# Optimization experiments

Hardware: AMD Instinct MI355X
Metric: run time of the kernel (lower is better)

## Reference

```python
import jax, jax.numpy as jnp
import numpy as np

B, T, D, H, L, C = 64, 512, 256, 1024, 2, 128


def setup_inputs() -> dict:
    key = jax.random.key(0)
    ks = jax.random.split(key, 11)
    s = 0.05
    return {
        "x": jax.random.normal(ks[0], (B, T, D), dtype=jnp.float32),
        "W_ih0": jax.random.normal(ks[1], (4 * H, D), dtype=jnp.float32) * s,
        "W_hh0": jax.random.normal(ks[2], (4 * H, H), dtype=jnp.float32) * s,
        "b_ih0": jax.random.normal(ks[3], (4 * H,), dtype=jnp.float32) * s,
        "b_hh0": jax.random.normal(ks[4], (4 * H,), dtype=jnp.float32) * s,
        "W_ih1": jax.random.normal(ks[5], (4 * H, H), dtype=jnp.float32) * s,
        "W_hh1": jax.random.normal(ks[6], (4 * H, H), dtype=jnp.float32) * s,
        "b_ih1": jax.random.normal(ks[7], (4 * H,), dtype=jnp.float32) * s,
        "b_hh1": jax.random.normal(ks[8], (4 * H,), dtype=jnp.float32) * s,
        "W_fc": jax.random.normal(ks[9], (C, H), dtype=jnp.float32) * s,
        "b_fc": jax.random.normal(ks[10], (C,), dtype=jnp.float32) * s,
    }


def _lstm_cell(inp, h, c, Wi, Wh, bi, bh):
    # PyTorch LSTMCell: gates ordered i, f, g, o
    gates = inp @ Wi.T + bi + h @ Wh.T + bh  # [B, 4H]
    i, f, g, o = jnp.split(gates, 4, axis=-1)
    c_new = jax.nn.sigmoid(f) * c + jax.nn.sigmoid(i) * jnp.tanh(g)
    h_new = jax.nn.sigmoid(o) * jnp.tanh(c_new)
    return h_new, c_new


def reference(x, W_ih0, W_hh0, b_ih0, b_hh0, W_ih1, W_hh1, b_ih1, b_hh1, W_fc, b_fc):
    b = x.shape[0]
    h0 = jnp.zeros((b, H), x.dtype)
    init = (h0, h0, h0, h0)  # (h_l0, c_l0, h_l1, c_l1)

    def step(carry, x_t):
        h0_, c0_, h1_, c1_ = carry
        h0n, c0n = _lstm_cell(x_t, h0_, c0_, W_ih0, W_hh0, b_ih0, b_hh0)
        h1n, c1n = _lstm_cell(h0n, h1_, c1_, W_ih1, W_hh1, b_ih1, b_hh1)
        return (h0n, c0n, h1n, c1n), None

    xt = jnp.swapaxes(x, 0, 1)  # [T, B, D]
    (h0f, c0f, h1f, c1f), _ = jax.lax.scan(step, init, xt)
    return h1f @ W_fc.T + b_fc  # [B, num_classes]
```

## Files before the change

### kernel.cpp

```cpp
#include <hip/hip_runtime.h>
#include <hip/hip_bf16.h>

#define B_ 64
#define T_ 512
#define D_ 256
#define H_ 1024
#define RING 64
#define PS 260

typedef __attribute__((ext_vector_type(8))) short short8;
typedef __attribute__((ext_vector_type(4))) float floatx4;

__device__ __forceinline__ unsigned short f2bf(float f){
  unsigned u = __builtin_bit_cast(unsigned, f);
  u = (u + 0x7fffu + ((u >> 16) & 1u)) >> 16;
  return (unsigned short)u;
}

__device__ __forceinline__ short8 pack8(floatx4 a, floatx4 b){
  short8 r;
  r[0]=(short)f2bf(a[0]); r[1]=(short)f2bf(a[1]); r[2]=(short)f2bf(a[2]); r[3]=(short)f2bf(a[3]);
  r[4]=(short)f2bf(b[0]); r[5]=(short)f2bf(b[1]); r[6]=(short)f2bf(b[2]); r[7]=(short)f2bf(b[3]);
  return r;
}

__device__ __forceinline__ float sigm(float v){ return 1.f/(1.f+__expf(-v)); }
__device__ __forceinline__ float tanh_f(float v){ return 1.f - 2.f/(1.f+__expf(2.f*v)); }

__device__ __forceinline__ void gpoll(const unsigned long long* watch, unsigned tgt0, unsigned tgt1){
  if (!(tgt0 | tgt1)) return;
  long g = 0;
  for (;;){
    unsigned long long v = __hip_atomic_load(watch, __ATOMIC_RELAXED, __HIP_MEMORY_SCOPE_AGENT);
    unsigned v0 = (unsigned)v, v1 = (unsigned)(v >> 32);
    if (__all(v0 >= tgt0 && v1 >= tgt1)) break;
    if (++g > (1L<<24)) break;
  }
}

__device__ __forceinline__ void lspin(unsigned* flag, unsigned tgt){
  long g = 0;
  while (__hip_atomic_load(flag, __ATOMIC_RELAXED, __HIP_MEMORY_SCOPE_WORKGROUP) < tgt){
    if (++g > (1L<<24)) break;
  }
}


template<int LAYER>
__device__ __forceinline__ void run_lstm(
    const float* __restrict__ x,
    const float* __restrict__ Wi, const float* __restrict__ Wh,
    const float* __restrict__ bi, const float* __restrict__ bh,
    unsigned* seq, unsigned short* h0h, unsigned short* h1h, float* h1f,
    int jbase, int j, int half,
    float* partial , float* c_st , float* biasv ,
    unsigned* rdy)
{
  constexpr int KTOT = LAYER ? 2048 : 1280;
  constexpr int KW   = KTOT/8;
  constexpr int NK   = KW/32;
  constexpr int KA   = LAYER ? 1024 : 256;

  const int tid  = threadIdx.x;
  const int wave = tid >> 6;
  const int lane = tid & 63;
  const int ksl  = wave;
  const int n15  = lane & 15;
  const int kq   = (lane >> 4) * 8;

  short8 bfr[4][NK];
  #pragma unroll
  for (int nt = 0; nt < 4; nt++){
    int n   = nt*16 + n15;
    int row = (n >> 4)*H_ + jbase + (n & 15);
    #pragma unroll
    for (int ks = 0; ks < NK; ks++){
      int k = ksl*KW + ks*32 + kq;
      const float* s = (k < KA) ? (Wi + (size_t)row*KA + k)
                                : (Wh + (size_t)row*H_ + (k - KA));
      bfr[nt][ks] = pack8(*(const floatx4*)s, *(const floatx4*)(s + 4));
    }
  }
  if (tid < 64){
    int col = (tid >> 4)*H_ + jbase + (tid & 15);
    biasv[tid] = bi[col] + bh[col];
  }
  c_st[tid & 511] = 0.f;
  if (tid == 0){ rdy[0] = 0u; }
  __syncthreads();

  const unsigned long long* watch =
      (const unsigned long long*)seq + (size_t)(LAYER*2 + half)*512 + lane;
  unsigned* post0 = seq + (size_t)(0*2 + half)*1024 + (size_t)j*2 + LAYER;
  unsigned* post1 = seq + (size_t)(1*2 + half)*1024 + (size_t)j*2 + LAYER;

  for (int t = 0; t < T_; t++){
    floatx4 xraw[LAYER ? 1 : NK][2][2];
    if constexpr (LAYER == 0){
      #pragma unroll
      for (int ks = 0; ks < NK; ks++){
        const int kb = ksl*KW + ks*32;
        if (kb < D_){
          const int kk = kb + kq;
          #pragma unroll
          for (int mt = 0; mt < 2; mt++){
            const float* xs = x + ((size_t)(half*32 + mt*16 + n15)*T_ + t)*D_ + kk;
            xraw[ks][mt][0] = *(const floatx4*)xs;
            xraw[ks][mt][1] = *(const floatx4*)(xs + 4);
          }
        }
      }
    }

    if (wave == 0){
      unsigned tgt0, tgt1;
      if (LAYER == 0){
        tgt0 = (unsigned)t;
        tgt1 = (t >= RING) ? (unsigned)(t - RING + 1) : 0u;
      } else {
        tgt0 = (unsigned)(t + 1);
        tgt1 = (unsigned)t;
      }
      gpoll(watch, tgt0, tgt1);
      if (lane == 0) __hip_atomic_store(&rdy[0], (unsigned)(t + 1),
                                        __ATOMIC_RELAXED, __HIP_MEMORY_SCOPE_WORKGROUP);
    } else {
      lspin(&rdy[0], (unsigned)(t + 1));
    }
    __builtin_amdgcn_sched_barrier(0);

    floatx4 acc[2][4];
    #pragma unroll
    for (int mt = 0; mt < 2; mt++)
      #pragma unroll
      for (int nt = 0; nt < 4; nt++)
        acc[mt][nt] = (floatx4)0.f;

    const unsigned short* h0t = h0h + ((size_t)((LAYER ? t : (t-1)) & (RING-1)) << 16);
    const unsigned short* h1t = h1h + ((size_t)((t-1) & (RING-1)) << 16);

    #pragma unroll
    for (int ks = 0; ks < NK; ks++){
      const int kb = ksl*KW + ks*32;
      if (kb >= KA && t == 0) continue;
      const int kk = kb + kq;
      short8 afr[2];
      if constexpr (LAYER == 0){
        if (kb < D_){
          #pragma unroll
          for (int mt = 0; mt < 2; mt++)
            afr[mt] = pack8(xraw[ks][mt][0], xraw[ks][mt][1]);
        } else {
          const int hk = kk - D_;
          const unsigned short* p = h0t + ((hk >> 4) << 10) + (hk & 15);
          #pragma unroll
          for (int mt = 0; mt < 2; mt++)
            afr[mt] = *(const short8*)(p + ((half*32 + mt*16 + n15) << 4));
        }
      } else {
        const int hk = (kb < 1024) ? kk : (kk - 1024);
        const unsigned short* sb = (kb < 1024) ? h0t : h1t;
        const unsigned short* p = sb + ((hk >> 4) << 10) + (hk & 15);
        #pragma unroll
        for (int mt = 0; mt < 2; mt++)
          afr[mt] = *(const short8*)(p + ((half*32 + mt*16 + n15) << 4));
      }
      #pragma unroll
      for (int mt = 0; mt < 2; mt++)
        #pragma unroll
        for (int nt = 0; nt < 4; nt++)
          acc[mt][nt] = __builtin_amdgcn_mfma_f32_16x16x32_bf16(afr[mt], bfr[nt][ks], acc[mt][nt], 0, 0, 0);
    }

    #pragma unroll
    for (int mt = 0; mt < 2; mt++)
      #pragma unroll
      for (int nt = 0; nt < 4; nt++){
        int n  = nt*16 + n15;
        int b0 = mt*16 + (lane >> 4)*4;
        *(floatx4*)(partial + (size_t)n*PS + ksl*32 + b0) = acc[mt][nt];
      }
    __syncthreads();

    {
      int b = tid >> 4, jj = tid & 15;
      float g[4];
      #pragma unroll
      for (int q = 0; q < 4; q++){
        const float* p = partial + (size_t)(q*16 + jj)*PS + b;
        float s = biasv[q*16 + jj];
        #pragma unroll
        for (int ss = 0; ss < 8; ss++) s += p[ss*32];
        g[q] = s;
      }
      float co = c_st[tid];
      float si = sigm(g[0]), sf = sigm(g[1]), tg = tanh_f(g[2]), so = sigm(g[3]);
      float cn = sf*co + si*tg;
      float hn = so*tanh_f(cn);
      c_st[tid] = cn;
      unsigned hb = (unsigned)f2bf(hn);
      unsigned ob = (unsigned)__shfl_xor((int)hb, 1, 64);
      if (!(jj & 1)){
        unsigned pk = hb | (ob << 16);
        unsigned short* dst = (LAYER ? h1h : h0h)
                            + ((size_t)(t & (RING-1)) << 16)
                            + ((size_t)j << 10) + ((size_t)(half*32 + b) << 4) + jj;
        __hip_atomic_store((unsigned*)dst, pk, __ATOMIC_RELAXED, __HIP_MEMORY_SCOPE_AGENT);
      }
      if (LAYER == 1 && t == T_-1)
        h1f[(size_t)(half*32 + b)*H_ + jbase + jj] = hn;
    }
    __syncthreads();
    if (tid == 0){
      __hip_atomic_store(post0, (unsigned)(t + 1), __ATOMIC_RELAXED, __HIP_MEMORY_SCOPE_AGENT);
      __hip_atomic_store(post1, (unsigned)(t + 1), __ATOMIC_RELAXED, __HIP_MEMORY_SCOPE_AGENT);
    }
  }
}

__global__ __launch_bounds__(512, 2) void lstm_pk(
    const float* __restrict__ x,
    const float* __restrict__ Wih0, const float* __restrict__ Whh0,
    const float* __restrict__ bih0, const float* __restrict__ bhh0,
    const float* __restrict__ Wih1, const float* __restrict__ Whh1,
    const float* __restrict__ bih1, const float* __restrict__ bhh1,
    char* __restrict__ ws)
{
  __shared__ __align__(16) float partial[64*PS];
  __shared__ float c_st[512];
  __shared__ float biasv[64];
  __shared__ unsigned rdy[1];

  unsigned* seq       = (unsigned*)ws;
  unsigned short* h0h = (unsigned short*)(ws + (1<<20));
  unsigned short* h1h = (unsigned short*)(ws + (1<<20) + RING*B_*H_*2);
  float* h1f          = (float*)(ws + (1<<20) + 2*(size_t)RING*B_*H_*2);

  const int bid = blockIdx.x;
  if (bid < 128){
    run_lstm<0>(x, Wih0, Whh0, bih0, bhh0, seq, h0h, h1h, h1f,
                (bid & 63)*16, bid & 63, bid >> 6, partial, c_st, biasv, rdy);
  } else {
    const int r = bid - 128;
    run_lstm<1>(x, Wih1, Whh1, bih1, bhh1, seq, h0h, h1h, h1f,
                (r & 63)*16, r & 63, r >> 6, partial, c_st, biasv, rdy);
  }
}

__global__ __launch_bounds__(128) void fc_k(
    const float* __restrict__ h1f, const float* __restrict__ Wfc,
    const float* __restrict__ bfc, float* __restrict__ out)
{
  __shared__ float hv[1024];
  int b = blockIdx.x, c = threadIdx.x;
  for (int i = c; i < 1024; i += 128) hv[i] = h1f[(size_t)b*1024 + i];
  __syncthreads();
  const floatx4* w4 = (const floatx4*)(Wfc + (size_t)c*1024);
  const floatx4* h4 = (const floatx4*)hv;
  float acc = 0.f;
  #pragma unroll 8
  for (int k = 0; k < 256; k++){
    floatx4 wv = w4[k];
    floatx4 hh = h4[k];
    acc += wv[0]*hh[0] + wv[1]*hh[1] + wv[2]*hh[2] + wv[3]*hh[3];
  }
  out[(size_t)b*128 + c] = acc + bfc[c];
}

extern "C" void kernel_launch(void* const* d_in, const int* in_sizes, int n_in,
                              void* d_out, int out_size, void* d_ws, size_t ws_size,
                              hipStream_t stream)
{
  const float* x    = (const float*)d_in[0];
  const float* Wih0 = (const float*)d_in[1];
  const float* Whh0 = (const float*)d_in[2];
  const float* bih0 = (const float*)d_in[3];
  const float* bhh0 = (const float*)d_in[4];
  const float* Wih1 = (const float*)d_in[5];
  const float* Whh1 = (const float*)d_in[6];
  const float* bih1 = (const float*)d_in[7];
  const float* bhh1 = (const float*)d_in[8];
  const float* Wfc  = (const float*)d_in[9];
  const float* bfc  = (const float*)d_in[10];

  hipMemsetAsync(d_ws, 0, 4*4096, stream);

  lstm_pk<<<256, 512, 0, stream>>>(x, Wih0, Whh0, bih0, bhh0, Wih1, Whh1, bih1, bhh1, (char*)d_ws);

  const float* h1f = (const float*)((char*)d_ws + (1<<20) + 2*(size_t)RING*B_*H_*2);
  fc_k<<<64, 128, 0, stream>>>(h1f, Wfc, bfc, (float*)d_out);
}
```

Before: 3.342 ms.

## Per-wave polling on dependency slices and split K to overlap waiting with compute

The old scheme had wave 0 poll global flags and release the other waves through a shared-memory flag. Now each wave polls only the producer flags for its own K slice. The K split is reorganised so each wave's slice maps to a known set of producer blocks. Work that does not depend on the awaited data (the input-x MFMA for layer 0, the own-layer h1 MFMA for layer 1) is issued before the poll, so waiting overlaps compute. Flag storage is compacted to one interleaved array, with cached seen values and a speculative prefetch of flags, at the cost of more global polling traffic and more complex ordering reasoning.

```diff
diff --git a/kernel.cpp b/kernel.cpp
--- a/kernel.cpp
+++ b/kernel.cpp
@@ -27,24 +27,20 @@
 __device__ __forceinline__ float sigm(float v){ return 1.f/(1.f+__expf(-v)); }
 __device__ __forceinline__ float tanh_f(float v){ return 1.f - 2.f/(1.f+__expf(2.f*v)); }
 
-__device__ __forceinline__ void gpoll(const unsigned long long* watch, unsigned tgt0, unsigned tgt1){
-  if (!(tgt0 | tgt1)) return;
+__device__ __forceinline__ void gpoll(const unsigned long long* watch,
+                                      unsigned& seen0, unsigned& seen1,
+                                      unsigned tgt0, unsigned tgt1){
+  if (__all(seen0 >= tgt0 && seen1 >= tgt1)) return;
   long g = 0;
   for (;;){
     unsigned long long v = __hip_atomic_load(watch, __ATOMIC_RELAXED, __HIP_MEMORY_SCOPE_AGENT);
     unsigned v0 = (unsigned)v, v1 = (unsigned)(v >> 32);
-    if (__all(v0 >= tgt0 && v1 >= tgt1)) break;
+    seen0 = v0 > seen0 ? v0 : seen0;
+    seen1 = v1 > seen1 ? v1 : seen1;
+    if (__all(seen0 >= tgt0 && seen1 >= tgt1)) break;
     if (++g > (1L<<24)) break;
   }
 }
-
-__device__ __forceinline__ void lspin(unsigned* flag, unsigned tgt){
-  long g = 0;
-  while (__hip_atomic_load(flag, __ATOMIC_RELAXED, __HIP_MEMORY_SCOPE_WORKGROUP) < tgt){
-    if (++g > (1L<<24)) break;
-  }
-}
-
 
 template<int LAYER>
 __device__ __forceinline__ void run_lstm(
@@ -53,18 +49,14 @@
     const float* __restrict__ bi, const float* __restrict__ bh,
     unsigned* seq, unsigned short* h0h, unsigned short* h1h, float* h1f,
     int jbase, int j, int half,
-    float* partial , float* c_st , float* biasv ,
-    unsigned* rdy)
-{
-  constexpr int KTOT = LAYER ? 2048 : 1280;
-  constexpr int KW   = KTOT/8;
-  constexpr int NK   = KW/32;
-  constexpr int KA   = LAYER ? 1024 : 256;
+    float* partial , float* c_st , float* biasv )
+{
+  constexpr int NK = LAYER ? 8 : 5;
+  constexpr int KA = LAYER ? 1024 : 256;
 
   const int tid  = threadIdx.x;
   const int wave = tid >> 6;
   const int lane = tid & 63;
-  const int ksl  = wave;
   const int n15  = lane & 15;
   const int kq   = (lane >> 4) * 8;
 
@@ -75,7 +67,8 @@
     int row = (n >> 4)*H_ + jbase + (n & 15);
     #pragma unroll
     for (int ks = 0; ks < NK; ks++){
-      int k = ksl*KW + ks*32 + kq;
+      int k = (LAYER ? (ks < 4 ? 1024 + wave*128 + ks*32 : wave*128 + (ks-4)*32)
+                     : (ks == 0 ? wave*32 : 256 + wave*128 + (ks-1)*32)) + kq;
       const float* s = (k < KA) ? (Wi + (size_t)row*KA + k)
                                 : (Wh + (size_t)row*H_ + (k - KA));
       bfr[nt][ks] = pack8(*(const floatx4*)s, *(const floatx4*)(s + 4));
@@ -86,48 +79,28 @@
     biasv[tid] = bi[col] + bh[col];
   }
   c_st[tid & 511] = 0.f;
-  if (tid == 0){ rdy[0] = 0u; }
   __syncthreads();
 
   const unsigned long long* watch =
-      (const unsigned long long*)seq + (size_t)(LAYER*2 + half)*512 + lane;
-  unsigned* post0 = seq + (size_t)(0*2 + half)*1024 + (size_t)j*2 + LAYER;
-  unsigned* post1 = seq + (size_t)(1*2 + half)*1024 + (size_t)j*2 + LAYER;
+      (const unsigned long long*)seq + (size_t)(half*64 + wave*8 + (lane & 7));
+
+  unsigned seen0 = 0, seen1 = 0;
+  unsigned long long vf = 0;
 
   for (int t = 0; t < T_; t++){
-    floatx4 xraw[LAYER ? 1 : NK][2][2];
+    { unsigned p0 = (unsigned)vf, p1 = (unsigned)(vf >> 32);
+      seen0 = p0 > seen0 ? p0 : seen0;
+      seen1 = p1 > seen1 ? p1 : seen1; }
+
+    floatx4 xr[2][2];
     if constexpr (LAYER == 0){
       #pragma unroll
-      for (int ks = 0; ks < NK; ks++){
-        const int kb = ksl*KW + ks*32;
-        if (kb < D_){
-          const int kk = kb + kq;
-          #pragma unroll
-          for (int mt = 0; mt < 2; mt++){
-            const float* xs = x + ((size_t)(half*32 + mt*16 + n15)*T_ + t)*D_ + kk;
-            xraw[ks][mt][0] = *(const floatx4*)xs;
-            xraw[ks][mt][1] = *(const floatx4*)(xs + 4);
-          }
-        }
-      }
-    }
-
-    if (wave == 0){
-      unsigned tgt0, tgt1;
-      if (LAYER == 0){
-        tgt0 = (unsigned)t;
-        tgt1 = (t >= RING) ? (unsigned)(t - RING + 1) : 0u;
-      } else {
-        tgt0 = (unsigned)(t + 1);
-        tgt1 = (unsigned)t;
-      }
-      gpoll(watch, tgt0, tgt1);
-      if (lane == 0) __hip_atomic_store(&rdy[0], (unsigned)(t + 1),
-                                        __ATOMIC_RELAXED, __HIP_MEMORY_SCOPE_WORKGROUP);
-    } else {
-      lspin(&rdy[0], (unsigned)(t + 1));
-    }
-    __builtin_amdgcn_sched_barrier(0);
+      for (int mt = 0; mt < 2; mt++){
+        const float* xs = x + ((size_t)(half*32 + mt*16 + n15)*T_ + t)*D_ + wave*32 + kq;
+        xr[mt][0] = *(const floatx4*)xs;
+        xr[mt][1] = *(const floatx4*)(xs + 4);
+      }
+    }
 
     floatx4 acc[2][4];
     #pragma unroll
@@ -139,37 +112,72 @@
     const unsigned short* h0t = h0h + ((size_t)((LAYER ? t : (t-1)) & (RING-1)) << 16);
     const unsigned short* h1t = h1h + ((size_t)((t-1) & (RING-1)) << 16);
 
-    #pragma unroll
-    for (int ks = 0; ks < NK; ks++){
-      const int kb = ksl*KW + ks*32;
-      if (kb >= KA && t == 0) continue;
-      const int kk = kb + kq;
-      short8 afr[2];
-      if constexpr (LAYER == 0){
-        if (kb < D_){
-          #pragma unroll
-          for (int mt = 0; mt < 2; mt++)
-            afr[mt] = pack8(xraw[ks][mt][0], xraw[ks][mt][1]);
-        } else {
-          const int hk = kk - D_;
+    if constexpr (LAYER == 0){
+      {
+        short8 afr0 = pack8(xr[0][0], xr[0][1]);
+        short8 afr1 = pack8(xr[1][0], xr[1][1]);
+        #pragma unroll
+        for (int nt = 0; nt < 4; nt++){
+          acc[0][nt] = __builtin_amdgcn_mfma_f32_16x16x32_bf16(afr0, bfr[nt][0], acc[0][nt], 0, 0, 0);
+          acc[1][nt] = __builtin_amdgcn_mfma_f32_16x16x32_bf16(afr1, bfr[nt][0], acc[1][nt], 0, 0, 0);
+        }
+      }
+      __builtin_amdgcn_sched_barrier(0);
+      gpoll(watch, seen0, seen1, (unsigned)t,
+            (t >= RING) ? (unsigned)(t - RING + 1) : 0u);
+      __builtin_amdgcn_sched_barrier(0);
+      if (t > 0){
+        #pragma unroll
+        for (int ks = 1; ks < 5; ks++){
+          const int hk = wave*128 + (ks-1)*32 + kq;
           const unsigned short* p = h0t + ((hk >> 4) << 10) + (hk & 15);
+          short8 afr[2];
           #pragma unroll
           for (int mt = 0; mt < 2; mt++)
             afr[mt] = *(const short8*)(p + ((half*32 + mt*16 + n15) << 4));
+          #pragma unroll
+          for (int mt = 0; mt < 2; mt++)
+            #pragma unroll
+            for (int nt = 0; nt < 4; nt++)
+              acc[mt][nt] = __builtin_amdgcn_mfma_f32_16x16x32_bf16(afr[mt], bfr[nt][ks], acc[mt][nt], 0, 0, 0);
         }
-      } else {
-        const int hk = (kb < 1024) ? kk : (kk - 1024);
-        const unsigned short* sb = (kb < 1024) ? h0t : h1t;
-        const unsigned short* p = sb + ((hk >> 4) << 10) + (hk & 15);
+      }
+    } else {
+      gpoll(watch, seen0, seen1, 0u, (unsigned)t);
+      __builtin_amdgcn_sched_barrier(0);
+      if (t > 0){
+        #pragma unroll
+        for (int ks = 0; ks < 4; ks++){
+          const int hk = wave*128 + ks*32 + kq;
+          const unsigned short* p = h1t + ((hk >> 4) << 10) + (hk & 15);
+          short8 afr[2];
+          #pragma unroll
+          for (int mt = 0; mt < 2; mt++)
+            afr[mt] = *(const short8*)(p + ((half*32 + mt*16 + n15) << 4));
+          #pragma unroll
+          for (int mt = 0; mt < 2; mt++)
+            #pragma unroll
+            for (int nt = 0; nt < 4; nt++)
+              acc[mt][nt] = __builtin_amdgcn_mfma_f32_16x16x32_bf16(afr[mt], bfr[nt][ks], acc[mt][nt], 0, 0, 0);
+        }
+      }
+      __builtin_amdgcn_sched_barrier(0);
+      gpoll(watch, seen0, seen1, (unsigned)(t + 1), 0u);
+      __builtin_amdgcn_sched_barrier(0);
+      #pragma unroll
+      for (int ks = 4; ks < 8; ks++){
+        const int hk = wave*128 + (ks-4)*32 + kq;
+        const unsigned short* p = h0t + ((hk >> 4) << 10) + (hk & 15);
+        short8 afr[2];
         #pragma unroll
         for (int mt = 0; mt < 2; mt++)
           afr[mt] = *(const short8*)(p + ((half*32 + mt*16 + n15) << 4));
-      }
-      #pragma unroll
-      for (int mt = 0; mt < 2; mt++)
-        #pragma unroll
-        for (int nt = 0; nt < 4; nt++)
-          acc[mt][nt] = __builtin_amdgcn_mfma_f32_16x16x32_bf16(afr[mt], bfr[nt][ks], acc[mt][nt], 0, 0, 0);
+        #pragma unroll
+        for (int mt = 0; mt < 2; mt++)
+          #pragma unroll
+          for (int nt = 0; nt < 4; nt++)
+            acc[mt][nt] = __builtin_amdgcn_mfma_f32_16x16x32_bf16(afr[mt], bfr[nt][ks], acc[mt][nt], 0, 0, 0);
+      }
     }
 
     #pragma unroll
@@ -178,7 +186,7 @@
       for (int nt = 0; nt < 4; nt++){
         int n  = nt*16 + n15;
         int b0 = mt*16 + (lane >> 4)*4;
-        *(floatx4*)(partial + (size_t)n*PS + ksl*32 + b0) = acc[mt][nt];
+        *(floatx4*)(partial + (size_t)n*PS + wave*32 + b0) = acc[mt][nt];
       }
     __syncthreads();
 
@@ -210,11 +218,11 @@
       if (LAYER == 1 && t == T_-1)
         h1f[(size_t)(half*32 + b)*H_ + jbase + jj] = hn;
     }
+    vf = __hip_atomic_load(watch, __ATOMIC_RELAXED, __HIP_MEMORY_SCOPE_AGENT);
     __syncthreads();
-    if (tid == 0){
-      __hip_atomic_store(post0, (unsigned)(t + 1), __ATOMIC_RELAXED, __HIP_MEMORY_SCOPE_AGENT);
-      __hip_atomic_store(post1, (unsigned)(t + 1), __ATOMIC_RELAXED, __HIP_MEMORY_SCOPE_AGENT);
-    }
+    if (tid == 0)
+      __hip_atomic_store(seq + (size_t)(half*64 + j)*2 + LAYER, (unsigned)(t + 1),
+                         __ATOMIC_RELAXED, __HIP_MEMORY_SCOPE_AGENT);
   }
 }
 
@@ -229,7 +237,6 @@
   __shared__ __align__(16) float partial[64*PS];
   __shared__ float c_st[512];
   __shared__ float biasv[64];
-  __shared__ unsigned rdy[1];
 
   unsigned* seq       = (unsigned*)ws;
   unsigned short* h0h = (unsigned short*)(ws + (1<<20));
@@ -239,11 +246,11 @@
   const int bid = blockIdx.x;
   if (bid < 128){
     run_lstm<0>(x, Wih0, Whh0, bih0, bhh0, seq, h0h, h1h, h1f,
-                (bid & 63)*16, bid & 63, bid >> 6, partial, c_st, biasv, rdy);
+                (bid & 63)*16, bid & 63, bid >> 6, partial, c_st, biasv);
   } else {
     const int r = bid - 128;
     run_lstm<1>(x, Wih1, Whh1, bih1, bhh1, seq, h0h, h1h, h1f,
-                (r & 63)*16, r & 63, r >> 6, partial, c_st, biasv, rdy);
+                (r & 63)*16, r & 63, r >> 6, partial, c_st, biasv);
   }
 }
 
@@ -283,7 +290,7 @@
   const float* Wfc  = (const float*)d_in[9];
   const float* bfc  = (const float*)d_in[10];
 
-  hipMemsetAsync(d_ws, 0, 4*4096, stream);
+  hipMemsetAsync(d_ws, 0, 4096, stream);
 
   lstm_pk<<<256, 512, 0, stream>>>(x, Wih0, Whh0, bih0, bhh0, Wih1, Whh1, bih1, bhh1, (char*)d_ws);
 
```

Measured after the change: 3.472 ms. 1.04x slower.
